# Kernel tuning notes

Hardware: AMD Instinct MI355X
Metric: run time of the kernel (lower is better)

Reference implementation:

```python
import jax, jax.numpy as jnp
import numpy as np

E = 256      # emb_size
H = 100      # ff_sim hidden
B, TQ, TK = 16, 128, 128


def setup_inputs() -> dict:
    key = jax.random.key(0)
    ks = jax.random.split(key, 8)
    queries = jax.random.normal(ks[0], (B, TQ, E), dtype=jnp.float32)
    keys = jax.random.normal(ks[1], (B, TK, E), dtype=jnp.float32)
    query_masks = jnp.ones((B, TQ), dtype=jnp.float32)
    key_masks = jnp.ones((B, TK), dtype=jnp.float32)
    # xavier_uniform bounds: sqrt(6/(fan_in+fan_out))
    def xavier(k, shape):
        fan_out, fan_in = shape
        lim = np.sqrt(6.0 / (fan_in + fan_out))
        return jax.random.uniform(k, shape, jnp.float32, -lim, lim)
    W1 = xavier(ks[2], (H, 2 * E))          # linear_ff_sim[0].weight
    b1 = jnp.zeros((H,), dtype=jnp.float32)  # linear_ff_sim[0].bias
    W2 = xavier(ks[3], (1, H))              # linear_ff_sim[2].weight (no bias)
    Wlast = xavier(ks[4], (E, 2 * E))       # linear_last.weight
    blast = jnp.zeros((E,), dtype=jnp.float32)
    return {"queries": queries, "keys": keys, "query_masks": query_masks,
            "key_masks": key_masks, "W1": W1, "b1": b1, "W2": W2,
            "Wlast": Wlast, "blast": blast}


def reference(queries, keys, query_masks, key_masks, W1, b1, W2, Wlast, blast):
    # forward calls attention_fc(keys, queries, key_masks, query_masks):
    #   attn queries = keys,  attn keys = queries,
    #   attn query_masks = key_masks, attn key_masks = query_masks.
    e = queries.shape[-1]
    # Additive-attention MLP score, decomposed: cat([keys_i, queries_j]) @ W1^T
    #   = keys_i @ W1[:, :E]^T + queries_j @ W1[:, E:]^T
    a = jnp.einsum('bie,he->bih', keys, W1[:, :e])      # [B,Tk,H]
    c = jnp.einsum('bje,he->bjh', queries, W1[:, e:])   # [B,Tq,H]
    h = jnp.tanh(a[:, :, None, :] + c[:, None, :, :] + b1)  # [B,Tk,Tq,H]
    sim = jnp.einsum('bijh,h->bij', h, W2[0])           # [B,Tk,Tq]
    neg = jnp.asarray(-2.0 ** 32 + 1, sim.dtype)
    sim = jnp.where(query_masks[:, None, :] == 0, neg, sim)
    sim = jax.nn.softmax(sim, axis=-1)
    sim = sim * key_masks[:, :, None]
    keys_attn = jnp.einsum('bij,bje->bie', sim, queries)  # [B,Tk,E]
    feature_mul = keys_attn * keys
    d = keys_attn - keys
    feature_sub = d * d
    feature_last = jnp.concatenate([feature_mul, feature_sub], axis=-1)  # [B,Tk,2E]
    return jax.nn.relu(jnp.einsum('bif,ef->bie', feature_last, Wlast) + blast)
```

## Files before the change

### kernel.cpp

```cpp
#include <hip/hip_runtime.h>


namespace {
constexpr int B  = 16;
constexpr int TQ = 128;
constexpr int TK = 128;
constexpr int E  = 256;
constexpr int H  = 100;
constexpr int HP = 112;
constexpr int G  = 8;
constexpr float SC = 2.8853900817779268f;
}

typedef __attribute__((ext_vector_type(8))) short short8;
typedef __attribute__((ext_vector_type(4))) float f32x4;

__device__ __forceinline__ unsigned short f2bf(float f) {
  unsigned u = __builtin_bit_cast(unsigned, f);
  u = (u + 0x7FFFu + ((u >> 16) & 1u)) >> 16;
  return (unsigned short)u;
}
__device__ __forceinline__ unsigned pk2(float x, float y) {
  return (unsigned)f2bf(x) | ((unsigned)f2bf(y) << 16);
}

__global__ __launch_bounds__(256) void prep_mfma(
    const float* __restrict__ queries, const float* __restrict__ keys,
    const float* __restrict__ W1, const float* __restrict__ b1,
    const float* __restrict__ Wlast,
    float* __restrict__ A, float* __restrict__ C,
    unsigned short* __restrict__ Wb) {
  __shared__ short Bs[112 * 264];
  __shared__ short As[16 * 264];
  const int t  = threadIdx.x;
  const int m0 = blockIdx.x * 16;
  const bool isA = (m0 < B * TK);
  const int koff = isA ? 0 : 256;
  float* dst = isA ? (A + (size_t)m0 * HP)
                   : (C + (size_t)(m0 - B * TK) * HP);

  {
    const int base = blockIdx.x * 512 + t * 2;
    float2 w = *(const float2*)(Wlast + base);
    *(unsigned*)(Wb + base) = pk2(w.x, w.y);
  }
  #pragma unroll
  for (int i = 0; i < 14; ++i) {
    const int idx = i * 256 + t;
    const int h = idx >> 5, seg = idx & 31;
    uint4 o = make_uint4(0u, 0u, 0u, 0u);
    if (h < H) {
      const float4* p = (const float4*)(W1 + (size_t)h * 512 + koff + seg * 8);
      float4 u = p[0], v = p[1];
      o = make_uint4(pk2(u.x, u.y), pk2(u.z, u.w), pk2(v.x, v.y), pk2(v.z, v.w));
    }
    *(uint4*)(Bs + h * 264 + seg * 8) = o;
  }
  #pragma unroll
  for (int i = 0; i < 2; ++i) {
    const int idx = i * 256 + t;
    const int r = idx >> 5, seg = idx & 31;
    const float* src = isA ? (keys + (size_t)(m0 + r) * E)
                           : (queries + (size_t)(m0 - B * TK + r) * E);
    const float4* p = (const float4*)(src + seg * 8);
    float4 u = p[0], v = p[1];
    *(uint4*)(As + r * 264 + seg * 8) =
        make_uint4(pk2(u.x, u.y), pk2(u.z, u.w), pk2(v.x, v.y), pk2(v.z, v.w));
  }
  __syncthreads();

  const int wave = t >> 6, lane = t & 63;
  const int m = lane & 15, kq = lane >> 4;
  const int nt0 = wave, nt1 = wave + 4;
  f32x4 acc0 = {0.f, 0.f, 0.f, 0.f}, acc1 = {0.f, 0.f, 0.f, 0.f};

  #pragma unroll
  for (int kc = 0; kc < 8; ++kc) {
    short8 a = *(const short8*)(As + m * 264 + kc * 32 + kq * 8);
    short8 bv0 = *(const short8*)(Bs + (nt0 * 16 + m) * 264 + kc * 32 + kq * 8);
    acc0 = __builtin_amdgcn_mfma_f32_16x16x32_bf16(a, bv0, acc0, 0, 0, 0);
    if (nt1 < 7) {
      short8 bv1 = *(const short8*)(Bs + (nt1 * 16 + m) * 264 + kc * 32 + kq * 8);
      acc1 = __builtin_amdgcn_mfma_f32_16x16x32_bf16(a, bv1, acc1, 0, 0, 0);
    }
  }

  const int rbase = (lane >> 4) * 4;
  {
    const int h = nt0 * 16 + m;
    const float bias = (isA && h < H) ? b1[h] : 0.0f;
    #pragma unroll
    for (int r = 0; r < 4; ++r)
      dst[(size_t)(rbase + r) * HP + h] = (acc0[r] + bias) * SC;
  }
  if (nt1 < 7) {
    const int h = nt1 * 16 + m;
    const float bias = (isA && h < H) ? b1[h] : 0.0f;
    #pragma unroll
    for (int r = 0; r < 4; ++r)
      dst[(size_t)(rbase + r) * HP + h] = (acc1[r] + bias) * SC;
  }
}

__global__ __launch_bounds__(512) void attn_gemm(
    const float* __restrict__ queries, const float* __restrict__ keys,
    const float* __restrict__ qmask, const float* __restrict__ kmask,
    const float* __restrict__ W2, const float* __restrict__ blast,
    const float* __restrict__ A, const float* __restrict__ C,
    const unsigned short* __restrict__ Wb, float* __restrict__ out) {
  __shared__ float a_s[G * HP];
  __shared__ float w2s[HP];
  __shared__ float qm[TQ];
  __shared__ float simP[G * 512];
  __shared__ float pL[G * TQ];
  __shared__ short featL[16 * 520];

  const int t   = threadIdx.x;
  const int blk = blockIdx.x;
  const int b   = blk >> 4;
  const int i0  = (blk & 15) * G;

  if (t < G * HP / 4)
    ((float4*)a_s)[t] = ((const float4*)(A + ((size_t)b * TK + i0) * HP))[t];
  if (t < HP) w2s[t] = (t < H) ? W2[t] : 0.0f;
  if (t < TQ) qm[t]  = qmask[b * TQ + t];
  #pragma unroll
  for (int i = 0; i < 2; ++i) {
    int idx = t + i * 512;
    if (idx < 520) ((uint4*)(featL + 8 * 520))[idx] = make_uint4(0u, 0u, 0u, 0u);
  }
  __syncthreads();

  const int j = t & (TQ - 1);
  const int q = t >> 7;
  float4 cr[7], wr[7];
  float wsum = 0.0f;
  {
    const float4* c4 = (const float4*)(C + ((size_t)b * TQ + j) * HP + q * 28);
    const float4* w4 = (const float4*)w2s + q * 7;
    #pragma unroll
    for (int k = 0; k < 7; ++k) {
      cr[k] = c4[k];
      wr[k] = w4[k];
      wsum += wr[k].x + wr[k].y + wr[k].z + wr[k].w;
    }
  }
  {
    const float4* a4p = (const float4*)a_s + q * 7;
    #pragma unroll
    for (int g = 0; g < G; ++g) {
      float s = 0.0f;
      #pragma unroll
      for (int k = 0; k < 7; ++k) {
        float4 a4 = a4p[g * 28 + k];
        s = fmaf(wr[k].x, __builtin_amdgcn_rcpf(exp2f(a4.x + cr[k].x) + 1.0f), s);
        s = fmaf(wr[k].y, __builtin_amdgcn_rcpf(exp2f(a4.y + cr[k].y) + 1.0f), s);
        s = fmaf(wr[k].z, __builtin_amdgcn_rcpf(exp2f(a4.z + cr[k].z) + 1.0f), s);
        s = fmaf(wr[k].w, __builtin_amdgcn_rcpf(exp2f(a4.w + cr[k].w) + 1.0f), s);
      }
      simP[g * 512 + t] = wsum - 2.0f * s;
    }
  }
  __syncthreads();

  {
    const int g = t >> 6, lane = t & 63;
    const float* sp = simP + g * 512;
    float sv0 = sp[lane]      + sp[128 + lane]      + sp[256 + lane]      + sp[384 + lane];
    float sv1 = sp[lane + 64] + sp[128 + lane + 64] + sp[256 + lane + 64] + sp[384 + lane + 64];
    if (qm[lane] == 0.0f)      sv0 = -4294967295.0f;
    if (qm[lane + 64] == 0.0f) sv1 = -4294967295.0f;
    float p0 = __expf(sv0), p1 = __expf(sv1);
    float s = p0 + p1;
    #pragma unroll
    for (int off = 1; off < 64; off <<= 1) s += __shfl_xor(s, off, 64);
    float inv = __builtin_amdgcn_rcpf(s);
    pL[g * TQ + lane]      = p0 * inv;
    pL[g * TQ + lane + 64] = p1 * inv;
  }
  __syncthreads();

  {
    const int e = t & 255, gh = t >> 8;
    float ka[4] = {0.f, 0.f, 0.f, 0.f};
    const float* qb = queries + (size_t)b * TQ * E + e;
    const float4* p4 = (const float4*)pL + (gh * 4) * 32;
    for (int j4 = 0; j4 < TQ / 4; ++j4) {
      float4 pv[4];
      #pragma unroll
      for (int gg = 0; gg < 4; ++gg) pv[gg] = p4[gg * 32 + j4];
      #pragma unroll
      for (int c = 0; c < 4; ++c) {
        float qv = qb[(size_t)(j4 * 4 + c) * E];
        #pragma unroll
        for (int gg = 0; gg < 4; ++gg)
          ka[gg] = fmaf(((const float*)&pv[gg])[c], qv, ka[gg]);
      }
    }
    #pragma unroll
    for (int gg = 0; gg < 4; ++gg) {
      const int g = gh * 4 + gg;
      const float kmv = kmask[b * TK + i0 + g];
      const float kav = ka[gg] * kmv;
      const float kv  = keys[((size_t)b * TK + i0 + g) * E + e];
      featL[g * 520 + e]     = (short)f2bf(kav * kv);
      float d = kav - kv;
      featL[g * 520 + E + e] = (short)f2bf(d * d);
    }
  }
  __syncthreads();

  {
    const int wave = t >> 6, lane = t & 63;
    const int m = lane & 15, kq = lane >> 4;
    f32x4 acc[2] = {{0.f, 0.f, 0.f, 0.f}, {0.f, 0.f, 0.f, 0.f}};
    #pragma unroll
    for (int kc = 0; kc < 16; ++kc) {
      short8 a = *(const short8*)(featL + m * 520 + kc * 32 + kq * 8);
      #pragma unroll
      for (int nt = 0; nt < 2; ++nt) {
        const int ncol = wave * 32 + nt * 16 + m;
        short8 bf = *(const short8*)(Wb + (size_t)ncol * 512 + kc * 32 + kq * 8);
        acc[nt] = __builtin_amdgcn_mfma_f32_16x16x32_bf16(a, bf, acc[nt], 0, 0, 0);
      }
    }
    const int rbase = (lane >> 4) * 4;
    if (rbase < 8) {
      #pragma unroll
      for (int nt = 0; nt < 2; ++nt) {
        const int ncol = wave * 32 + nt * 16 + (lane & 15);
        const float bl = blast[ncol];
        #pragma unroll
        for (int r = 0; r < 4; ++r)
          out[((size_t)b * TK + i0 + rbase + r) * E + ncol] =
              fmaxf(acc[nt][r] + bl, 0.0f);
      }
    }
  }
}

extern "C" void kernel_launch(void* const* d_in, const int* in_sizes, int n_in,
                              void* d_out, int out_size, void* d_ws, size_t ws_size,
                              hipStream_t stream) {
  (void)in_sizes; (void)n_in; (void)out_size; (void)ws_size;
  const float* queries = (const float*)d_in[0];
  const float* keys    = (const float*)d_in[1];
  const float* qmask   = (const float*)d_in[2];
  const float* kmask   = (const float*)d_in[3];
  const float* W1      = (const float*)d_in[4];
  const float* b1      = (const float*)d_in[5];
  const float* W2      = (const float*)d_in[6];
  const float* Wlast   = (const float*)d_in[7];
  const float* blast   = (const float*)d_in[8];
  float* out = (float*)d_out;

  float* A = (float*)d_ws;
  float* C = A + (size_t)B * TK * HP;
  unsigned short* Wb = (unsigned short*)(C + (size_t)B * TQ * HP);

  prep_mfma<<<dim3(256), dim3(256), 0, stream>>>(
      queries, keys, W1, b1, Wlast, A, C, Wb);
  attn_gemm<<<dim3(B * (TK / G)), dim3(512), 0, stream>>>(
      queries, keys, qmask, kmask, W2, blast, A, C, Wb, out);
}
```

Baseline: 100.4 us.

## Fuse projection prep into attention kernel, recompute per-block projections in LDS

Merges the two kernels into one. Each block now converts W1 to bf16 in shared memory, computes its own 8 key-row projections and all 128 query-row projections with MFMA, and keeps them in a unioned LDS region instead of round-tripping A/C through global workspace. Wlast is also converted to bf16 on the fly inside the final GEMM rather than being pre-packed. This removes one launch and the global stores and reloads of the intermediates. In exchange every block redundantly recomputes the full query projection and reconverts W1 and Wlast, so total compute and L2 traffic go up.

```diff
diff --git a/kernel.cpp b/kernel.cpp
--- a/kernel.cpp
+++ b/kernel.cpp
@@ -9,7 +9,8 @@
 constexpr int H  = 100;
 constexpr int HP = 112;
 constexpr int G  = 8;
-constexpr float SC = 2.8853900817779268f;
+constexpr int CLS = 116;
+constexpr float SCALE = 2.8853900817779268f;
 }
 
 typedef __attribute__((ext_vector_type(8))) short short8;
@@ -23,111 +24,115 @@
 __device__ __forceinline__ unsigned pk2(float x, float y) {
   return (unsigned)f2bf(x) | ((unsigned)f2bf(y) << 16);
 }
-
-__global__ __launch_bounds__(256) void prep_mfma(
+union U16 { uint4 u; short8 s; };
+__device__ __forceinline__ short8 pack8(float4 a, float4 b) {
+  U16 t;
+  t.u = make_uint4(pk2(a.x, a.y), pk2(a.z, a.w), pk2(b.x, b.y), pk2(b.z, b.w));
+  return t.s;
+}
+
+__global__ __launch_bounds__(512) void nns_fused(
     const float* __restrict__ queries, const float* __restrict__ keys,
+    const float* __restrict__ qmask, const float* __restrict__ kmask,
     const float* __restrict__ W1, const float* __restrict__ b1,
-    const float* __restrict__ Wlast,
-    float* __restrict__ A, float* __restrict__ C,
-    unsigned short* __restrict__ Wb) {
-  __shared__ short Bs[112 * 264];
-  __shared__ short As[16 * 264];
-  const int t  = threadIdx.x;
-  const int m0 = blockIdx.x * 16;
-  const bool isA = (m0 < B * TK);
-  const int koff = isA ? 0 : 256;
-  float* dst = isA ? (A + (size_t)m0 * HP)
-                   : (C + (size_t)(m0 - B * TK) * HP);
-
-  {
-    const int base = blockIdx.x * 512 + t * 2;
-    float2 w = *(const float2*)(Wlast + base);
-    *(unsigned*)(Wb + base) = pk2(w.x, w.y);
-  }
+    const float* __restrict__ W2, const float* __restrict__ Wlast,
+    const float* __restrict__ blast, float* __restrict__ out) {
+  union Region {
+    short ws[112 * 264];
+    float cl[128 * CLS];
+    struct {
+      float simP[8 * 512];
+      float pL[8 * 128];
+      short featL[16 * 520];
+    } p;
+  };
+  __shared__ Region R;
+  __shared__ float a_s[G * HP];
+  __shared__ float w2s[HP];
+  __shared__ float qm[TQ];
+
+  const int t    = threadIdx.x;
+  const int blk  = blockIdx.x;
+  const int b    = blk >> 4;
+  const int i0   = (blk & 15) * G;
+  const int wave = t >> 6, lane = t & 63;
+  const int m    = lane & 15, kq = lane >> 4;
+
   #pragma unroll
-  for (int i = 0; i < 14; ++i) {
-    const int idx = i * 256 + t;
+  for (int i = 0; i < 7; ++i) {
+    const int idx = i * 512 + t;
     const int h = idx >> 5, seg = idx & 31;
     uint4 o = make_uint4(0u, 0u, 0u, 0u);
     if (h < H) {
-      const float4* p = (const float4*)(W1 + (size_t)h * 512 + koff + seg * 8);
-      float4 u = p[0], v = p[1];
+      const float4* p4 = (const float4*)(W1 + (size_t)h * 512 + seg * 8);
+      float4 u = p4[0], v = p4[1];
       o = make_uint4(pk2(u.x, u.y), pk2(u.z, u.w), pk2(v.x, v.y), pk2(v.z, v.w));
     }
-    *(uint4*)(Bs + h * 264 + seg * 8) = o;
-  }
-  #pragma unroll
-  for (int i = 0; i < 2; ++i) {
-    const int idx = i * 256 + t;
-    const int r = idx >> 5, seg = idx & 31;
-    const float* src = isA ? (keys + (size_t)(m0 + r) * E)
-                           : (queries + (size_t)(m0 - B * TK + r) * E);
-    const float4* p = (const float4*)(src + seg * 8);
-    float4 u = p[0], v = p[1];
-    *(uint4*)(As + r * 264 + seg * 8) =
-        make_uint4(pk2(u.x, u.y), pk2(u.z, u.w), pk2(v.x, v.y), pk2(v.z, v.w));
-  }
-  __syncthreads();
-
-  const int wave = t >> 6, lane = t & 63;
-  const int m = lane & 15, kq = lane >> 4;
-  const int nt0 = wave, nt1 = wave + 4;
-  f32x4 acc0 = {0.f, 0.f, 0.f, 0.f}, acc1 = {0.f, 0.f, 0.f, 0.f};
-
-  #pragma unroll
-  for (int kc = 0; kc < 8; ++kc) {
-    short8 a = *(const short8*)(As + m * 264 + kc * 32 + kq * 8);
-    short8 bv0 = *(const short8*)(Bs + (nt0 * 16 + m) * 264 + kc * 32 + kq * 8);
-    acc0 = __builtin_amdgcn_mfma_f32_16x16x32_bf16(a, bv0, acc0, 0, 0, 0);
-    if (nt1 < 7) {
-      short8 bv1 = *(const short8*)(Bs + (nt1 * 16 + m) * 264 + kc * 32 + kq * 8);
-      acc1 = __builtin_amdgcn_mfma_f32_16x16x32_bf16(a, bv1, acc1, 0, 0, 0);
-    }
-  }
-
-  const int rbase = (lane >> 4) * 4;
-  {
-    const int h = nt0 * 16 + m;
-    const float bias = (isA && h < H) ? b1[h] : 0.0f;
-    #pragma unroll
-    for (int r = 0; r < 4; ++r)
-      dst[(size_t)(rbase + r) * HP + h] = (acc0[r] + bias) * SC;
-  }
-  if (nt1 < 7) {
-    const int h = nt1 * 16 + m;
-    const float bias = (isA && h < H) ? b1[h] : 0.0f;
-    #pragma unroll
-    for (int r = 0; r < 4; ++r)
-      dst[(size_t)(rbase + r) * HP + h] = (acc1[r] + bias) * SC;
-  }
-}
-
-__global__ __launch_bounds__(512) void attn_gemm(
-    const float* __restrict__ queries, const float* __restrict__ keys,
-    const float* __restrict__ qmask, const float* __restrict__ kmask,
-    const float* __restrict__ W2, const float* __restrict__ blast,
-    const float* __restrict__ A, const float* __restrict__ C,
-    const unsigned short* __restrict__ Wb, float* __restrict__ out) {
-  __shared__ float a_s[G * HP];
-  __shared__ float w2s[HP];
-  __shared__ float qm[TQ];
-  __shared__ float simP[G * 512];
-  __shared__ float pL[G * TQ];
-  __shared__ short featL[16 * 520];
-
-  const int t   = threadIdx.x;
-  const int blk = blockIdx.x;
-  const int b   = blk >> 4;
-  const int i0  = (blk & 15) * G;
-
-  if (t < G * HP / 4)
-    ((float4*)a_s)[t] = ((const float4*)(A + ((size_t)b * TK + i0) * HP))[t];
+    *(uint4*)(R.ws + h * 264 + seg * 8) = o;
+  }
   if (t < HP) w2s[t] = (t < H) ? W2[t] : 0.0f;
   if (t < TQ) qm[t]  = qmask[b * TQ + t];
+  __syncthreads();
+
+  if (wave < 7) {
+    const int krow = b * TK + min(i0 + m, TK - 1);
+    f32x4 acc = {0.f, 0.f, 0.f, 0.f};
+    #pragma unroll
+    for (int kc = 0; kc < 8; ++kc) {
+      const float4* kp = (const float4*)(keys + (size_t)krow * E + kc * 32 + kq * 8);
+      short8 af = pack8(kp[0], kp[1]);
+      short8 bf = *(const short8*)(R.ws + (wave * 16 + m) * 264 + kc * 32 + kq * 8);
+      acc = __builtin_amdgcn_mfma_f32_16x16x32_bf16(af, bf, acc, 0, 0, 0);
+    }
+    const int h  = wave * 16 + m;
+    const float bias = (h < H) ? b1[h] : 0.0f;
+    const int lr = (lane >> 4) * 4;
+    if (lr < 8) {
+      #pragma unroll
+      for (int r = 0; r < 4; ++r)
+        a_s[(lr + r) * HP + h] = (acc[r] + bias) * SCALE;
+    }
+  }
+  __syncthreads();
+
   #pragma unroll
-  for (int i = 0; i < 2; ++i) {
-    int idx = t + i * 512;
-    if (idx < 520) ((uint4*)(featL + 8 * 520))[idx] = make_uint4(0u, 0u, 0u, 0u);
+  for (int i = 0; i < 7; ++i) {
+    const int idx = i * 512 + t;
+    const int h = idx >> 5, seg = idx & 31;
+    uint4 o = make_uint4(0u, 0u, 0u, 0u);
+    if (h < H) {
+      const float4* p4 = (const float4*)(W1 + (size_t)h * 512 + 256 + seg * 8);
+      float4 u = p4[0], v = p4[1];
+      o = make_uint4(pk2(u.x, u.y), pk2(u.z, u.w), pk2(v.x, v.y), pk2(v.z, v.w));
+    }
+    *(uint4*)(R.ws + h * 264 + seg * 8) = o;
+  }
+  __syncthreads();
+
+  {
+    f32x4 accc[7];
+    #pragma unroll
+    for (int nt = 0; nt < 7; ++nt) accc[nt] = f32x4{0.f, 0.f, 0.f, 0.f};
+    const int qrow = b * TQ + wave * 16 + m;
+    #pragma unroll
+    for (int kc = 0; kc < 8; ++kc) {
+      const float4* qp = (const float4*)(queries + (size_t)qrow * E + kc * 32 + kq * 8);
+      short8 af = pack8(qp[0], qp[1]);
+      #pragma unroll
+      for (int nt = 0; nt < 7; ++nt) {
+        short8 bf = *(const short8*)(R.ws + (nt * 16 + m) * 264 + kc * 32 + kq * 8);
+        accc[nt] = __builtin_amdgcn_mfma_f32_16x16x32_bf16(af, bf, accc[nt], 0, 0, 0);
+      }
+    }
+    __syncthreads();
+    const int jb = wave * 16 + (lane >> 4) * 4;
+    #pragma unroll
+    for (int nt = 0; nt < 7; ++nt) {
+      const int h = nt * 16 + m;
+      #pragma unroll
+      for (int r = 0; r < 4; ++r)
+        R.cl[(jb + r) * CLS + h] = accc[nt][r] * SCALE;
+    }
   }
   __syncthreads();
 
@@ -136,7 +141,7 @@
   float4 cr[7], wr[7];
   float wsum = 0.0f;
   {
-    const float4* c4 = (const float4*)(C + ((size_t)b * TQ + j) * HP + q * 28);
+    const float4* c4 = (const float4*)R.cl + j * (CLS / 4) + q * 7;
     const float4* w4 = (const float4*)w2s + q * 7;
     #pragma unroll
     for (int k = 0; k < 7; ++k) {
@@ -145,6 +150,13 @@
       wsum += wr[k].x + wr[k].y + wr[k].z + wr[k].w;
     }
   }
+  __syncthreads();
+
+  {
+    uint4* z = (uint4*)(R.p.featL + 8 * 520);
+    for (int i = t; i < 520; i += 512) z[i] = make_uint4(0u, 0u, 0u, 0u);
+  }
+
   {
     const float4* a4p = (const float4*)a_s + q * 7;
     #pragma unroll
@@ -158,16 +170,15 @@
         s = fmaf(wr[k].z, __builtin_amdgcn_rcpf(exp2f(a4.z + cr[k].z) + 1.0f), s);
         s = fmaf(wr[k].w, __builtin_amdgcn_rcpf(exp2f(a4.w + cr[k].w) + 1.0f), s);
       }
-      simP[g * 512 + t] = wsum - 2.0f * s;
-    }
-  }
-  __syncthreads();
-
-  {
-    const int g = t >> 6, lane = t & 63;
-    const float* sp = simP + g * 512;
-    float sv0 = sp[lane]      + sp[128 + lane]      + sp[256 + lane]      + sp[384 + lane];
-    float sv1 = sp[lane + 64] + sp[128 + lane + 64] + sp[256 + lane + 64] + sp[384 + lane + 64];
+      R.p.simP[g * 512 + t] = wsum - 2.0f * s;
+    }
+  }
+  __syncthreads();
+
+  {
+    const float* sp = R.p.simP + wave * 512;
+    float sv0 = sp[lane]      + sp[lane + 128] + sp[lane + 256] + sp[lane + 384];
+    float sv1 = sp[lane + 64] + sp[lane + 192] + sp[lane + 320] + sp[lane + 448];
     if (qm[lane] == 0.0f)      sv0 = -4294967295.0f;
     if (qm[lane + 64] == 0.0f) sv1 = -4294967295.0f;
     float p0 = __expf(sv0), p1 = __expf(sv1);
@@ -175,8 +186,8 @@
     #pragma unroll
     for (int off = 1; off < 64; off <<= 1) s += __shfl_xor(s, off, 64);
     float inv = __builtin_amdgcn_rcpf(s);
-    pL[g * TQ + lane]      = p0 * inv;
-    pL[g * TQ + lane + 64] = p1 * inv;
+    R.p.pL[wave * TQ + lane]      = p0 * inv;
+    R.p.pL[wave * TQ + lane + 64] = p1 * inv;
   }
   __syncthreads();
 
@@ -184,7 +195,7 @@
     const int e = t & 255, gh = t >> 8;
     float ka[4] = {0.f, 0.f, 0.f, 0.f};
     const float* qb = queries + (size_t)b * TQ * E + e;
-    const float4* p4 = (const float4*)pL + (gh * 4) * 32;
+    const float4* p4 = (const float4*)R.p.pL + (gh * 4) * 32;
     for (int j4 = 0; j4 < TQ / 4; ++j4) {
       float4 pv[4];
       #pragma unroll
@@ -203,32 +214,31 @@
       const float kmv = kmask[b * TK + i0 + g];
       const float kav = ka[gg] * kmv;
       const float kv  = keys[((size_t)b * TK + i0 + g) * E + e];
-      featL[g * 520 + e]     = (short)f2bf(kav * kv);
+      R.p.featL[g * 520 + e]     = (short)f2bf(kav * kv);
       float d = kav - kv;
-      featL[g * 520 + E + e] = (short)f2bf(d * d);
-    }
-  }
-  __syncthreads();
-
-  {
-    const int wave = t >> 6, lane = t & 63;
-    const int m = lane & 15, kq = lane >> 4;
+      R.p.featL[g * 520 + E + e] = (short)f2bf(d * d);
+    }
+  }
+  __syncthreads();
+
+  {
     f32x4 acc[2] = {{0.f, 0.f, 0.f, 0.f}, {0.f, 0.f, 0.f, 0.f}};
     #pragma unroll
     for (int kc = 0; kc < 16; ++kc) {
-      short8 a = *(const short8*)(featL + m * 520 + kc * 32 + kq * 8);
+      short8 a = *(const short8*)(R.p.featL + m * 520 + kc * 32 + kq * 8);
       #pragma unroll
       for (int nt = 0; nt < 2; ++nt) {
         const int ncol = wave * 32 + nt * 16 + m;
-        short8 bf = *(const short8*)(Wb + (size_t)ncol * 512 + kc * 32 + kq * 8);
-        acc[nt] = __builtin_amdgcn_mfma_f32_16x16x32_bf16(a, bf, acc[nt], 0, 0, 0);
+        const float4* wp = (const float4*)(Wlast + (size_t)ncol * 512 + kc * 32 + kq * 8);
+        short8 bfv = pack8(wp[0], wp[1]);
+        acc[nt] = __builtin_amdgcn_mfma_f32_16x16x32_bf16(a, bfv, acc[nt], 0, 0, 0);
       }
     }
     const int rbase = (lane >> 4) * 4;
     if (rbase < 8) {
       #pragma unroll
       for (int nt = 0; nt < 2; ++nt) {
-        const int ncol = wave * 32 + nt * 16 + (lane & 15);
+        const int ncol = wave * 32 + nt * 16 + m;
         const float bl = blast[ncol];
         #pragma unroll
         for (int r = 0; r < 4; ++r)
@@ -242,7 +252,7 @@
 extern "C" void kernel_launch(void* const* d_in, const int* in_sizes, int n_in,
                               void* d_out, int out_size, void* d_ws, size_t ws_size,
                               hipStream_t stream) {
-  (void)in_sizes; (void)n_in; (void)out_size; (void)ws_size;
+  (void)in_sizes; (void)n_in; (void)out_size; (void)d_ws; (void)ws_size;
   const float* queries = (const float*)d_in[0];
   const float* keys    = (const float*)d_in[1];
   const float* qmask   = (const float*)d_in[2];
@@ -254,12 +264,6 @@
   const float* blast   = (const float*)d_in[8];
   float* out = (float*)d_out;
 
-  float* A = (float*)d_ws;
-  float* C = A + (size_t)B * TK * HP;
-  unsigned short* Wb = (unsigned short*)(C + (size_t)B * TQ * HP);
-
-  prep_mfma<<<dim3(256), dim3(256), 0, stream>>>(
-      queries, keys, W1, b1, Wlast, A, C, Wb);
-  attn_gemm<<<dim3(B * (TK / G)), dim3(512), 0, stream>>>(
-      queries, keys, qmask, kmask, W2, blast, A, C, Wb, out);
-}
+  nns_fused<<<dim3(B * (TK / G)), dim3(512), 0, stream>>>(
+      queries, keys, qmask, kmask, W1, b1, W2, Wlast, blast, out);
+}
```

New measurement: 112.5 us. 12.0% more time.

## Split prep into bf16 conversion and per-wave GEMM, halve attention row group

Applied to the files above, without the earlier changes.

The fused prep kernel, which staged W1 in shared memory per block, is replaced by a separate bf16 conversion kernel and a small MFMA GEMM kernel where each wave computes one 16x16 tile straight from global bf16 data. The attention kernel now handles 4 key rows per block with 256 threads instead of 8 rows with 512, doubling the block count to 512 and raising occupancy. The intent is to drop redundant W1 conversion across blocks and balance work across CUs. In exchange it adds a third launch and extra workspace traffic, and the final GEMM in each block keeps only 4 of the 16 MFMA rows.

```diff
diff --git a/kernel.cpp b/kernel.cpp
--- a/kernel.cpp
+++ b/kernel.cpp
@@ -8,8 +8,8 @@
 constexpr int E  = 256;
 constexpr int H  = 100;
 constexpr int HP = 112;
-constexpr int G  = 8;
-constexpr float SC = 2.8853900817779268f;
+constexpr int G  = 4;
+constexpr float SCALE = 2.8853900817779268f;
 }
 
 typedef __attribute__((ext_vector_type(8))) short short8;
@@ -23,86 +23,70 @@
 __device__ __forceinline__ unsigned pk2(float x, float y) {
   return (unsigned)f2bf(x) | ((unsigned)f2bf(y) << 16);
 }
-
-__global__ __launch_bounds__(256) void prep_mfma(
+__device__ __forceinline__ uint4 pack8u(float4 a, float4 b) {
+  return make_uint4(pk2(a.x, a.y), pk2(a.z, a.w), pk2(b.x, b.y), pk2(b.z, b.w));
+}
+
+__global__ __launch_bounds__(256) void convert_bf16(
     const float* __restrict__ queries, const float* __restrict__ keys,
-    const float* __restrict__ W1, const float* __restrict__ b1,
-    const float* __restrict__ Wlast,
-    float* __restrict__ A, float* __restrict__ C,
+    const float* __restrict__ W1, const float* __restrict__ Wlast,
+    unsigned short* __restrict__ Xb, unsigned short* __restrict__ Wb1,
     unsigned short* __restrict__ Wb) {
-  __shared__ short Bs[112 * 264];
-  __shared__ short As[16 * 264];
-  const int t  = threadIdx.x;
-  const int m0 = blockIdx.x * 16;
-  const bool isA = (m0 < B * TK);
-  const int koff = isA ? 0 : 256;
-  float* dst = isA ? (A + (size_t)m0 * HP)
-                   : (C + (size_t)(m0 - B * TK) * HP);
-
-  {
-    const int base = blockIdx.x * 512 + t * 2;
-    float2 w = *(const float2*)(Wlast + base);
-    *(unsigned*)(Wb + base) = pk2(w.x, w.y);
-  }
-  #pragma unroll
-  for (int i = 0; i < 14; ++i) {
-    const int idx = i * 256 + t;
-    const int h = idx >> 5, seg = idx & 31;
+  const int blk = blockIdx.x, t = threadIdx.x;
+  if (blk < 512) {
+    const int idx = blk * 2048 + t * 8;
+    const int row = idx >> 8, e = idx & 255;
+    const float* src = (row < B * TK) ? keys + (size_t)row * E + e
+                                      : queries + (size_t)(row - B * TK) * E + e;
+    const float4* p4 = (const float4*)src;
+    *(uint4*)(Xb + idx) = pack8u(p4[0], p4[1]);
+  } else if (blk < 540) {
+    const int idx = (blk - 512) * 2048 + t * 8;
+    const int h = idx >> 9;
     uint4 o = make_uint4(0u, 0u, 0u, 0u);
     if (h < H) {
-      const float4* p = (const float4*)(W1 + (size_t)h * 512 + koff + seg * 8);
-      float4 u = p[0], v = p[1];
-      o = make_uint4(pk2(u.x, u.y), pk2(u.z, u.w), pk2(v.x, v.y), pk2(v.z, v.w));
-    }
-    *(uint4*)(Bs + h * 264 + seg * 8) = o;
-  }
-  #pragma unroll
-  for (int i = 0; i < 2; ++i) {
-    const int idx = i * 256 + t;
-    const int r = idx >> 5, seg = idx & 31;
-    const float* src = isA ? (keys + (size_t)(m0 + r) * E)
-                           : (queries + (size_t)(m0 - B * TK + r) * E);
-    const float4* p = (const float4*)(src + seg * 8);
-    float4 u = p[0], v = p[1];
-    *(uint4*)(As + r * 264 + seg * 8) =
-        make_uint4(pk2(u.x, u.y), pk2(u.z, u.w), pk2(v.x, v.y), pk2(v.z, v.w));
-  }
-  __syncthreads();
-
-  const int wave = t >> 6, lane = t & 63;
-  const int m = lane & 15, kq = lane >> 4;
-  const int nt0 = wave, nt1 = wave + 4;
-  f32x4 acc0 = {0.f, 0.f, 0.f, 0.f}, acc1 = {0.f, 0.f, 0.f, 0.f};
-
+      const float4* p4 = (const float4*)(W1 + idx);
+      o = pack8u(p4[0], p4[1]);
+    }
+    *(uint4*)(Wb1 + idx) = o;
+  } else {
+    const int idx = (blk - 540) * 2048 + t * 8;
+    const float4* p4 = (const float4*)(Wlast + idx);
+    *(uint4*)(Wb + idx) = pack8u(p4[0], p4[1]);
+  }
+}
+
+__global__ __launch_bounds__(256, 4) void prep_gemm(
+    const unsigned short* __restrict__ Xb, const unsigned short* __restrict__ Wb1,
+    const float* __restrict__ b1, float* __restrict__ A, float* __restrict__ C) {
+  const int t = threadIdx.x;
+  const int tid = blockIdx.x * 4 + (t >> 6);
+  const int mt = tid / 7, nt = tid % 7;
+  const int lane = t & 63, m = lane & 15, kq = lane >> 4;
+
+  const bool isA = (mt * 16 < B * TK);
+  const int koff = isA ? 0 : 256;
+
+  const unsigned short* ap = Xb + (size_t)(mt * 16 + m) * 256 + kq * 8;
+  const unsigned short* bp = Wb1 + (size_t)(nt * 16 + m) * 512 + koff + kq * 8;
+  f32x4 acc = {0.f, 0.f, 0.f, 0.f};
   #pragma unroll
   for (int kc = 0; kc < 8; ++kc) {
-    short8 a = *(const short8*)(As + m * 264 + kc * 32 + kq * 8);
-    short8 bv0 = *(const short8*)(Bs + (nt0 * 16 + m) * 264 + kc * 32 + kq * 8);
-    acc0 = __builtin_amdgcn_mfma_f32_16x16x32_bf16(a, bv0, acc0, 0, 0, 0);
-    if (nt1 < 7) {
-      short8 bv1 = *(const short8*)(Bs + (nt1 * 16 + m) * 264 + kc * 32 + kq * 8);
-      acc1 = __builtin_amdgcn_mfma_f32_16x16x32_bf16(a, bv1, acc1, 0, 0, 0);
-    }
-  }
-
+    short8 af = *(const short8*)(ap + kc * 32);
+    short8 bf = *(const short8*)(bp + kc * 32);
+    acc = __builtin_amdgcn_mfma_f32_16x16x32_bf16(af, bf, acc, 0, 0, 0);
+  }
+  const int h = nt * 16 + m;
+  const float bias = (isA && h < H) ? b1[h] : 0.0f;
+  float* dst = isA ? (A + (size_t)(mt * 16) * HP)
+                   : (C + (size_t)(mt * 16 - B * TK) * HP);
   const int rbase = (lane >> 4) * 4;
-  {
-    const int h = nt0 * 16 + m;
-    const float bias = (isA && h < H) ? b1[h] : 0.0f;
-    #pragma unroll
-    for (int r = 0; r < 4; ++r)
-      dst[(size_t)(rbase + r) * HP + h] = (acc0[r] + bias) * SC;
-  }
-  if (nt1 < 7) {
-    const int h = nt1 * 16 + m;
-    const float bias = (isA && h < H) ? b1[h] : 0.0f;
-    #pragma unroll
-    for (int r = 0; r < 4; ++r)
-      dst[(size_t)(rbase + r) * HP + h] = (acc1[r] + bias) * SC;
-  }
-}
-
-__global__ __launch_bounds__(512) void attn_gemm(
+  #pragma unroll
+  for (int r = 0; r < 4; ++r)
+    dst[(size_t)(rbase + r) * HP + h] = (acc[r] + bias) * SCALE;
+}
+
+__global__ __launch_bounds__(256, 4) void attn(
     const float* __restrict__ queries, const float* __restrict__ keys,
     const float* __restrict__ qmask, const float* __restrict__ kmask,
     const float* __restrict__ W2, const float* __restrict__ blast,
@@ -111,63 +95,64 @@
   __shared__ float a_s[G * HP];
   __shared__ float w2s[HP];
   __shared__ float qm[TQ];
-  __shared__ float simP[G * 512];
+  __shared__ float simP[G * 256];
   __shared__ float pL[G * TQ];
   __shared__ short featL[16 * 520];
 
-  const int t   = threadIdx.x;
-  const int blk = blockIdx.x;
-  const int b   = blk >> 4;
-  const int i0  = (blk & 15) * G;
+  const int t    = threadIdx.x;
+  const int blk  = blockIdx.x;
+  const int b    = blk >> 5;
+  const int i0   = (blk & 31) * G;
+  const int wave = t >> 6, lane = t & 63;
+  const int m    = lane & 15, kq = lane >> 4;
 
   if (t < G * HP / 4)
     ((float4*)a_s)[t] = ((const float4*)(A + ((size_t)b * TK + i0) * HP))[t];
   if (t < HP) w2s[t] = (t < H) ? W2[t] : 0.0f;
   if (t < TQ) qm[t]  = qmask[b * TQ + t];
-  #pragma unroll
-  for (int i = 0; i < 2; ++i) {
-    int idx = t + i * 512;
-    if (idx < 520) ((uint4*)(featL + 8 * 520))[idx] = make_uint4(0u, 0u, 0u, 0u);
-  }
-  __syncthreads();
-
-  const int j = t & (TQ - 1);
-  const int q = t >> 7;
-  float4 cr[7], wr[7];
-  float wsum = 0.0f;
-  {
-    const float4* c4 = (const float4*)(C + ((size_t)b * TQ + j) * HP + q * 28);
-    const float4* w4 = (const float4*)w2s + q * 7;
-    #pragma unroll
-    for (int k = 0; k < 7; ++k) {
-      cr[k] = c4[k];
-      wr[k] = w4[k];
-      wsum += wr[k].x + wr[k].y + wr[k].z + wr[k].w;
-    }
-  }
-  {
-    const float4* a4p = (const float4*)a_s + q * 7;
-    #pragma unroll
-    for (int g = 0; g < G; ++g) {
-      float s = 0.0f;
+  __syncthreads();
+
+  {
+    const int j  = t & 127;
+    const int h2 = t >> 7;
+    float acc[G] = {0.f, 0.f, 0.f, 0.f};
+    #pragma unroll
+    for (int pp = 0; pp < 2; ++pp) {
+      const int q = h2 * 2 + pp;
+      float4 cr[7], wr[7];
+      float wsum = 0.0f;
+      const float4* c4 = (const float4*)(C + ((size_t)b * TQ + j) * HP + q * 28);
+      const float4* w4 = (const float4*)w2s + q * 7;
       #pragma unroll
       for (int k = 0; k < 7; ++k) {
-        float4 a4 = a4p[g * 28 + k];
-        s = fmaf(wr[k].x, __builtin_amdgcn_rcpf(exp2f(a4.x + cr[k].x) + 1.0f), s);
-        s = fmaf(wr[k].y, __builtin_amdgcn_rcpf(exp2f(a4.y + cr[k].y) + 1.0f), s);
-        s = fmaf(wr[k].z, __builtin_amdgcn_rcpf(exp2f(a4.z + cr[k].z) + 1.0f), s);
-        s = fmaf(wr[k].w, __builtin_amdgcn_rcpf(exp2f(a4.w + cr[k].w) + 1.0f), s);
-      }
-      simP[g * 512 + t] = wsum - 2.0f * s;
-    }
-  }
-  __syncthreads();
-
-  {
-    const int g = t >> 6, lane = t & 63;
-    const float* sp = simP + g * 512;
-    float sv0 = sp[lane]      + sp[128 + lane]      + sp[256 + lane]      + sp[384 + lane];
-    float sv1 = sp[lane + 64] + sp[128 + lane + 64] + sp[256 + lane + 64] + sp[384 + lane + 64];
+        cr[k] = c4[k];
+        wr[k] = w4[k];
+        wsum += wr[k].x + wr[k].y + wr[k].z + wr[k].w;
+      }
+      const float4* a4p = (const float4*)a_s + q * 7;
+      #pragma unroll
+      for (int g = 0; g < G; ++g) {
+        float s = 0.0f;
+        #pragma unroll
+        for (int k = 0; k < 7; ++k) {
+          float4 a4 = a4p[g * 28 + k];
+          s = fmaf(wr[k].x, __builtin_amdgcn_rcpf(exp2f(a4.x + cr[k].x) + 1.0f), s);
+          s = fmaf(wr[k].y, __builtin_amdgcn_rcpf(exp2f(a4.y + cr[k].y) + 1.0f), s);
+          s = fmaf(wr[k].z, __builtin_amdgcn_rcpf(exp2f(a4.z + cr[k].z) + 1.0f), s);
+          s = fmaf(wr[k].w, __builtin_amdgcn_rcpf(exp2f(a4.w + cr[k].w) + 1.0f), s);
+        }
+        acc[g] += wsum - 2.0f * s;
+      }
+    }
+    #pragma unroll
+    for (int g = 0; g < G; ++g) simP[g * 256 + t] = acc[g];
+  }
+  __syncthreads();
+
+  {
+    const float* sp = simP + wave * 256;
+    float sv0 = sp[lane]      + sp[lane + 128];
+    float sv1 = sp[lane + 64] + sp[lane + 192];
     if (qm[lane] == 0.0f)      sv0 = -4294967295.0f;
     if (qm[lane + 64] == 0.0f) sv1 = -4294967295.0f;
     float p0 = __expf(sv0), p1 = __expf(sv1);
@@ -175,33 +160,32 @@
     #pragma unroll
     for (int off = 1; off < 64; off <<= 1) s += __shfl_xor(s, off, 64);
     float inv = __builtin_amdgcn_rcpf(s);
-    pL[g * TQ + lane]      = p0 * inv;
-    pL[g * TQ + lane + 64] = p1 * inv;
-  }
-  __syncthreads();
-
-  {
-    const int e = t & 255, gh = t >> 8;
-    float ka[4] = {0.f, 0.f, 0.f, 0.f};
+    pL[wave * TQ + lane]      = p0 * inv;
+    pL[wave * TQ + lane + 64] = p1 * inv;
+  }
+  __syncthreads();
+
+  {
+    const int e = t;
+    float ka[G] = {0.f, 0.f, 0.f, 0.f};
     const float* qb = queries + (size_t)b * TQ * E + e;
-    const float4* p4 = (const float4*)pL + (gh * 4) * 32;
+    const float4* p4 = (const float4*)pL;
     for (int j4 = 0; j4 < TQ / 4; ++j4) {
-      float4 pv[4];
-      #pragma unroll
-      for (int gg = 0; gg < 4; ++gg) pv[gg] = p4[gg * 32 + j4];
+      float4 pv[G];
+      #pragma unroll
+      for (int g = 0; g < G; ++g) pv[g] = p4[g * 32 + j4];
       #pragma unroll
       for (int c = 0; c < 4; ++c) {
         float qv = qb[(size_t)(j4 * 4 + c) * E];
         #pragma unroll
-        for (int gg = 0; gg < 4; ++gg)
-          ka[gg] = fmaf(((const float*)&pv[gg])[c], qv, ka[gg]);
-      }
-    }
-    #pragma unroll
-    for (int gg = 0; gg < 4; ++gg) {
-      const int g = gh * 4 + gg;
+        for (int g = 0; g < G; ++g)
+          ka[g] = fmaf(((const float*)&pv[g])[c], qv, ka[g]);
+      }
+    }
+    #pragma unroll
+    for (int g = 0; g < G; ++g) {
       const float kmv = kmask[b * TK + i0 + g];
-      const float kav = ka[gg] * kmv;
+      const float kav = ka[g] * kmv;
       const float kv  = keys[((size_t)b * TK + i0 + g) * E + e];
       featL[g * 520 + e]     = (short)f2bf(kav * kv);
       float d = kav - kv;
@@ -211,29 +195,27 @@
   __syncthreads();
 
   {
-    const int wave = t >> 6, lane = t & 63;
-    const int m = lane & 15, kq = lane >> 4;
-    f32x4 acc[2] = {{0.f, 0.f, 0.f, 0.f}, {0.f, 0.f, 0.f, 0.f}};
+    f32x4 acc[4];
+    #pragma unroll
+    for (int nt = 0; nt < 4; ++nt) acc[nt] = f32x4{0.f, 0.f, 0.f, 0.f};
     #pragma unroll
     for (int kc = 0; kc < 16; ++kc) {
       short8 a = *(const short8*)(featL + m * 520 + kc * 32 + kq * 8);
       #pragma unroll
-      for (int nt = 0; nt < 2; ++nt) {
-        const int ncol = wave * 32 + nt * 16 + m;
+      for (int nt = 0; nt < 4; ++nt) {
+        const int ncol = wave * 64 + nt * 16 + m;
         short8 bf = *(const short8*)(Wb + (size_t)ncol * 512 + kc * 32 + kq * 8);
         acc[nt] = __builtin_amdgcn_mfma_f32_16x16x32_bf16(a, bf, acc[nt], 0, 0, 0);
       }
     }
-    const int rbase = (lane >> 4) * 4;
-    if (rbase < 8) {
-      #pragma unroll
-      for (int nt = 0; nt < 2; ++nt) {
-        const int ncol = wave * 32 + nt * 16 + (lane & 15);
+    if ((lane >> 4) == 0) {
+      #pragma unroll
+      for (int nt = 0; nt < 4; ++nt) {
+        const int ncol = wave * 64 + nt * 16 + m;
         const float bl = blast[ncol];
         #pragma unroll
         for (int r = 0; r < 4; ++r)
-          out[((size_t)b * TK + i0 + rbase + r) * E + ncol] =
-              fmaxf(acc[nt][r] + bl, 0.0f);
+          out[((size_t)b * TK + i0 + r) * E + ncol] = fmaxf(acc[nt][r] + bl, 0.0f);
       }
     }
   }
@@ -256,10 +238,13 @@
 
   float* A = (float*)d_ws;
   float* C = A + (size_t)B * TK * HP;
-  unsigned short* Wb = (unsigned short*)(C + (size_t)B * TQ * HP);
-
-  prep_mfma<<<dim3(256), dim3(256), 0, stream>>>(
-      queries, keys, W1, b1, Wlast, A, C, Wb);
-  attn_gemm<<<dim3(B * (TK / G)), dim3(512), 0, stream>>>(
+  unsigned short* Wb1 = (unsigned short*)(C + (size_t)B * TQ * HP);
+  unsigned short* Wb  = Wb1 + (size_t)HP * 512;
+  unsigned short* Xb  = Wb + (size_t)E * 512;
+
+  convert_bf16<<<dim3(604), dim3(256), 0, stream>>>(
+      queries, keys, W1, Wlast, Xb, Wb1, Wb);
+  prep_gemm<<<dim3(448), dim3(256), 0, stream>>>(Xb, Wb1, b1, A, C);
+  attn<<<dim3(512), dim3(256), 0, stream>>>(
       queries, keys, qmask, kmask, W2, blast, A, C, Wb, out);
 }
```

Measured after the change: 107.7 us. +7.2%, slower.
